# Optimization experiments

Hardware: AMD Instinct MI355X
Metric: run time of the kernel (lower is better)

The kernel has to match this reference:

```python
import jax, jax.numpy as jnp
import numpy as np

B, L, E, H, CDIM = 512, 64, 256, 256, 64
NEG = -1e9  # stand-in for -inf mask fill (keeps grads nan-free; probs underflow to 0)
C_EXPL = 10.0  # tanh_exploration


def setup_inputs():
    key = jax.random.key(0)
    ks = jax.random.split(key, 24)
    rn = lambda k, s: jax.random.normal(k, s, jnp.float32) * 0.05
    return {
        'decoder_input': rn(ks[0], (B, E)),
        'embedded_inputs': rn(ks[1], (L, B, E)),
        'h0': rn(ks[2], (B, H)),
        'c0': rn(ks[3], (B, H)),
        'context': rn(ks[4], (L, B, H)),
        'courier_fea': rn(ks[5], (B, CDIM)),
        'init_mask': jnp.zeros((B, L), dtype=bool),
        # LSTMCell params (torch gate order i,f,g,o)
        'W_ih': rn(ks[6], (4 * H, E)), 'W_hh': rn(ks[7], (4 * H, H)),
        'b_ih': rn(ks[8], (4 * H,)), 'b_hh': rn(ks[9], (4 * H,)),
        # merge_linear
        'Wm': rn(ks[10], (H, H + CDIM)), 'bm': rn(ks[11], (H,)),
        # pointer attention
        'Wq_p': rn(ks[12], (H, H)), 'bq_p': rn(ks[13], (H,)),
        'Wr_p': rn(ks[14], (H, H)), 'br_p': rn(ks[15], (H,)),
        'v_p': rn(ks[16], (H,)),
        # glimpse attention
        'Wq_g': rn(ks[17], (H, H)), 'bq_g': rn(ks[18], (H,)),
        'Wr_g': rn(ks[19], (H, H)), 'br_g': rn(ks[20], (H,)),
        'v_g': rn(ks[21], (H,)),
    }


def _attn_scores(q_lin, e, v, use_tanh):
    # q_lin: [B,H], e: [B,H,L], v: [H] -> u: [B,L]
    u = jnp.einsum('h,bhl->bl', v, jnp.tanh(q_lin[:, :, None] + e))
    return C_EXPL * jnp.tanh(u) if use_tanh else u


def _forward(decoder_input, embedded_inputs, h0, c0, context, courier_fea,
             W_ih, W_hh, b_ih, b_hh, Wm, bm,
             Wq_p, bq_p, Wr_p, br_p, v_p,
             Wq_g, bq_g, Wr_g, br_g, v_g, init_mask):
    Ln, Bn = context.shape[0], context.shape[1]
    # conv1d(kernel=1) projection of encoder refs; constant over steps -> precompute
    e_g = jnp.einsum('oh,lbh->bol', Wr_g, context) + br_g[None, :, None]  # [B,H,L]
    e_p = jnp.einsum('oh,lbh->bol', Wr_p, context) + br_p[None, :, None]
    rows = jnp.arange(Bn)

    def update_mask(mask, sel):
        m = mask.at[rows, sel].set(True)
        all_true = m.all(axis=1)
        return m.at[:, -1].set(jnp.where(all_true, False, m[:, -1]))

    def step(carry, t):
        h, c, mask, idxs, x = carry
        mask = jnp.where(t == 0, mask, update_mask(mask, jnp.clip(idxs, 0)))
        # LSTMCell
        gates = x @ W_ih.T + b_ih + h @ W_hh.T + b_hh
        i_, f_, g_, o_ = jnp.split(gates, 4, axis=1)
        c = jax.nn.sigmoid(f_) * c + jax.nn.sigmoid(i_) * jnp.tanh(g_)
        h = jax.nn.sigmoid(o_) * jnp.tanh(c)
        # merge hidden with courier features
        gl = jnp.concatenate([h, courier_fea], axis=1) @ Wm.T + bm
        # one glimpse (n_glimpses=1), masked
        lg = _attn_scores(gl @ Wq_g.T + bq_g, e_g, v_g, use_tanh=False)
        lg = jnp.where(mask, NEG, lg)
        gl = jnp.einsum('bhl,bl->bh', e_g, jax.nn.softmax(lg, axis=1))
        # pointer logits (C*tanh), masked
        lp = _attn_scores(gl @ Wq_p.T + bq_p, e_p, v_p, use_tanh=True)
        lp = jnp.where(mask, NEG, lp)
        log_p = jax.nn.log_softmax(lp, axis=1)  # [B,L]
        new_idxs = jnp.argmax(log_p, axis=1).astype(jnp.int32)  # greedy decode
        new_x = embedded_inputs[new_idxs, rows, :]  # gather next input [B,E]
        return (h, c, mask, new_idxs, new_x), (log_p, new_idxs)

    init = (h0, c0, init_mask, jnp.full((Bn,), -1, jnp.int32), decoder_input)
    _, (log_ps, sels) = jax.lax.scan(step, init, jnp.arange(Ln))
    return jnp.swapaxes(log_ps, 0, 1), jnp.swapaxes(sels, 0, 1)  # [B,L,L], [B,L]


def reference(decoder_input, embedded_inputs, h0, c0, context, courier_fea, init_mask,
              W_ih, W_hh, b_ih, b_hh, Wm, bm,
              Wq_p, bq_p, Wr_p, br_p, v_p,
              Wq_g, bq_g, Wr_g, br_g, v_g):
    return _forward(decoder_input, embedded_inputs, h0, c0, context, courier_fea,
                    W_ih, W_hh, b_ih, b_hh, Wm, bm,
                    Wq_p, bq_p, Wr_p, br_p, v_p,
                    Wq_g, bq_g, Wr_g, br_g, v_g, init_mask)
```

## Files before the change

### kernel.cpp

```cpp
#include <hip/hip_runtime.h>
#include <cstdint>
#include <cstddef>

#define NEGV -1000000000.0f

__device__ __forceinline__ float fsigm(float x) {
  return 1.0f / (1.0f + __expf(-x));
}
__device__ __forceinline__ float ftanh(float x) {
  x = fminf(x, 30.0f);
  const float e = __expf(2.0f * x);
  return (e - 1.0f) / (e + 1.0f);
}

#define GLOAD_LDS16(gp, lp)                                             \
  __builtin_amdgcn_global_load_lds(                                     \
      (__attribute__((address_space(1))) void*)(gp),                    \
      (__attribute__((address_space(3))) void*)(lp), 16, 0, 0)

__global__ __launch_bounds__(256, 2) void gemm2_k(
    const float* __restrict__ A0, const float* __restrict__ W2,
    const float* __restrict__ b2, float* __restrict__ Cg,
    float* __restrict__ Cp)
{
  __shared__ float As[16][136];
  __shared__ float Ws[2][16][72];
  const int bm = blockIdx.x << 7;
  const int bn = blockIdx.y << 6;
  const int t  = threadIdx.x;
  const int ty = t >> 4, tx = t & 15;
  const int ar = t >> 1, ac = (t & 1) << 3;
  const int wr = t >> 2, wc = (t & 3) << 2;
  const float* arow = A0 + (size_t)(bm + ar) * 256 + ac;
  const float* w0row = W2 + (size_t)(bn + wr) * 256 + wc;
  const float* w1row = W2 + (size_t)(256 + bn + wr) * 256 + wc;
  float acc[2][8][4] = {};
  float4 a0 = *(const float4*)(arow + 0);
  float4 a1 = *(const float4*)(arow + 4);
  float4 wv0 = *(const float4*)(w0row + 0);
  float4 wv1 = *(const float4*)(w1row + 0);
  for (int k0 = 0; k0 < 256; k0 += 16) {
    As[ac + 0][ar] = a0.x; As[ac + 1][ar] = a0.y; As[ac + 2][ar] = a0.z; As[ac + 3][ar] = a0.w;
    As[ac + 4][ar] = a1.x; As[ac + 5][ar] = a1.y; As[ac + 6][ar] = a1.z; As[ac + 7][ar] = a1.w;
    Ws[0][wc + 0][wr] = wv0.x; Ws[0][wc + 1][wr] = wv0.y;
    Ws[0][wc + 2][wr] = wv0.z; Ws[0][wc + 3][wr] = wv0.w;
    Ws[1][wc + 0][wr] = wv1.x; Ws[1][wc + 1][wr] = wv1.y;
    Ws[1][wc + 2][wr] = wv1.z; Ws[1][wc + 3][wr] = wv1.w;
    __syncthreads();
    if (k0 < 240) {
      a0  = *(const float4*)(arow + k0 + 16);
      a1  = *(const float4*)(arow + k0 + 20);
      wv0 = *(const float4*)(w0row + k0 + 16);
      wv1 = *(const float4*)(w1row + k0 + 16);
    }
#pragma unroll
    for (int k = 0; k < 16; ++k) {
      const float4 a0v = *(const float4*)&As[k][ty << 3];
      const float4 a1v = *(const float4*)&As[k][(ty << 3) + 4];
      const float am[8] = {a0v.x, a0v.y, a0v.z, a0v.w, a1v.x, a1v.y, a1v.z, a1v.w};
#pragma unroll
      for (int s = 0; s < 2; ++s) {
        const float4 wv = *(const float4*)&Ws[s][k][tx << 2];
#pragma unroll
        for (int i = 0; i < 8; ++i) {
          acc[s][i][0] += am[i] * wv.x;
          acc[s][i][1] += am[i] * wv.y;
          acc[s][i][2] += am[i] * wv.z;
          acc[s][i][3] += am[i] * wv.w;
        }
      }
    }
    __syncthreads();
  }
  const int cn = bn + (tx << 2);
  const float4 bg = *(const float4*)(b2 + cn);
  const float4 bp = *(const float4*)(b2 + 256 + cn);
#pragma unroll
  for (int i = 0; i < 8; ++i) {
    const size_t row = ((size_t)(bm + (ty << 3) + i)) << 8;
    float4 o;
    o.x = acc[0][i][0] + bg.x; o.y = acc[0][i][1] + bg.y;
    o.z = acc[0][i][2] + bg.z; o.w = acc[0][i][3] + bg.w;
    *(float4*)(Cg + row + cn) = o;
    o.x = acc[1][i][0] + bp.x; o.y = acc[1][i][1] + bp.y;
    o.z = acc[1][i][2] + bp.z; o.w = acc[1][i][3] + bp.w;
    *(float4*)(Cp + row + cn) = o;
  }
}

__global__ __launch_bounds__(256) void gates_lstm_k(
    const float* __restrict__ x, const float* __restrict__ hin,
    const float* __restrict__ Wcat, const float* __restrict__ bcat,
    const float* __restrict__ cin, float* __restrict__ cnew,
    float* __restrict__ hnew)
{
  __shared__ __align__(16) float As[16][36];
  __shared__ __align__(16) float Ws[32][68];
  const int bn = blockIdx.x << 6;
  const int bm = blockIdx.y << 4;
  const int t  = threadIdx.x;
  const int ty = t >> 4, tx = t & 15;
  const int ar = t >> 4, ak = (t & 15) << 1;
  const int wr = t >> 2, wk = (t & 3) << 3;
  const float* wrow = Wcat + ((size_t)(bn + wr) << 9);
  const int arow = bm + ar;
  float acc0 = 0.f, acc1 = 0.f, acc2 = 0.f, acc3 = 0.f;
  for (int k0 = 0; k0 < 512; k0 += 32) {
    const int kk = k0 + ak;
    float2 av;
    if (kk < 256) av = *(const float2*)(x   + ((size_t)arow << 8) + kk);
    else          av = *(const float2*)(hin + ((size_t)arow << 8) + (kk - 256));
    const float4 w0 = *(const float4*)(wrow + k0 + wk);
    const float4 w1 = *(const float4*)(wrow + k0 + wk + 4);
    *(float2*)&As[ar][ak] = av;
    Ws[wk + 0][wr] = w0.x; Ws[wk + 1][wr] = w0.y; Ws[wk + 2][wr] = w0.z; Ws[wk + 3][wr] = w0.w;
    Ws[wk + 4][wr] = w1.x; Ws[wk + 5][wr] = w1.y; Ws[wk + 6][wr] = w1.z; Ws[wk + 7][wr] = w1.w;
    __syncthreads();
#pragma unroll
    for (int k = 0; k < 32; ++k) {
      const float a  = As[ty][k];
      const float4 w = *(const float4*)&Ws[k][tx << 2];
      acc0 += a * w.x; acc1 += a * w.y; acc2 += a * w.z; acc3 += a * w.w;
    }
    __syncthreads();
  }
  const float4 bb = *(const float4*)(bcat + bn + (tx << 2));
  const int jc = (bn >> 2) + tx;
  const int m  = bm + ty;
  const float ig = fsigm(acc0 + bb.x);
  const float fg = fsigm(acc1 + bb.y);
  const float gg = ftanh(acc2 + bb.z);
  const float og = fsigm(acc3 + bb.w);
  const float c  = fg * cin[(m << 8) + jc] + ig * gg;
  const float h  = og * ftanh(c);
  cnew[(m << 8) + jc] = c;
  hnew[(m << 8) + jc] = h;
}

__global__ __launch_bounds__(512) void step_attn_k(
    const float* __restrict__ h, const float* __restrict__ e2g,
    const float* __restrict__ e2p, const float* __restrict__ Wq1T4,
    const float* __restrict__ Wqp4, const float* __restrict__ qcour,
    const float* __restrict__ bqp, const float* __restrict__ vg,
    const float* __restrict__ vp, unsigned long long* __restrict__ mask,
    int* __restrict__ idxb, const float* __restrict__ emb,
    float* __restrict__ out_logp, float* __restrict__ out_sel,
    float* __restrict__ xb, int t)
{
  const int b = blockIdx.x, tid = threadIdx.x;
  __shared__ __align__(16) float hs[256], qgs[256], qps[256], gls[256];
  __shared__ __align__(16) float vgs[256], vps[256];
  __shared__ __align__(16) float glp[8][256];
  __shared__ __align__(16) float eps[64][256];
  __shared__ float us[64], mxs[8], zws[8];
  __shared__ unsigned long long ms;
  __shared__ int bsel;
  float* part = &glp[0][0];
  if (tid < 256) {
    hs[tid]  = h[(b << 8) + tid];
    vgs[tid] = vg[tid];
    vps[tid] = vp[tid];
  }
  if (tid == 0) {
    unsigned long long m = mask[b];
    if (t > 0) {
      int s = idxb[b]; if (s < 0) s = 0;
      m |= (1ULL << s);
      if (m == ~0ULL) m &= ~(1ULL << 63);
      mask[b] = m;
    }
    ms = m;
  }
  __syncthreads();
  const unsigned long long mm = ms;
  const int w = tid >> 6, lane = tid & 63;
  const int o = tid & 255, kh = tid >> 8;

  {
    const float* gb = e2g + ((size_t)b << 8) + (lane << 2);
#pragma unroll
    for (int li = 0; li < 8; ++li) {
      const int l = (w << 3) + li;
      GLOAD_LDS16(gb + ((size_t)l << 17), &eps[l][0]);
    }
  }

  {
    float acc = (kh == 0) ? qcour[(b << 8) + o] : 0.f;
    const float4* wp = (const float4*)Wq1T4 + o;
    const int kc0 = kh << 5;
#pragma unroll 8
    for (int kc = kc0; kc < kc0 + 32; ++kc) {
      const float4 wv = wp[kc << 8];
      const float4 h4 = *(const float4*)&hs[kc << 2];
      acc += wv.x * h4.x + wv.y * h4.y + wv.z * h4.z + wv.w * h4.w;
    }
    part[tid] = acc;
  }
  __syncthreads();
  if (tid < 256) qgs[tid] = part[tid] + part[tid + 256];
  __syncthreads();

  {
    const float4 q4 = *(const float4*)&qgs[lane << 2];
    const float4 v4 = *(const float4*)&vgs[lane << 2];
    float g0 = 0.f, g1 = 0.f, g2 = 0.f, g3 = 0.f;
    float mxw = -1e30f, zw = 0.f;
    for (int li = 0; li < 8; ++li) {
      const int l = (w << 3) + li;
      const float4 e4 = *(const float4*)&eps[l][lane << 2];
      float s = v4.x * ftanh(q4.x + e4.x) + v4.y * ftanh(q4.y + e4.y)
              + v4.z * ftanh(q4.z + e4.z) + v4.w * ftanh(q4.w + e4.w);
#pragma unroll
      for (int off = 32; off; off >>= 1) s += __shfl_xor(s, off, 64);
      if (!((mm >> l) & 1ULL)) {
        const float nm   = fmaxf(mxw, s);
        const float corr = __expf(mxw - nm);
        const float wl   = __expf(s - nm);
        zw = zw * corr + wl;
        g0 = g0 * corr + wl * e4.x; g1 = g1 * corr + wl * e4.y;
        g2 = g2 * corr + wl * e4.z; g3 = g3 * corr + wl * e4.w;
        mxw = nm;
      }
    }
    glp[w][(lane << 2) + 0] = g0; glp[w][(lane << 2) + 1] = g1;
    glp[w][(lane << 2) + 2] = g2; glp[w][(lane << 2) + 3] = g3;
    if (lane == 0) { mxs[w] = mxw; zws[w] = zw; }
  }
  __syncthreads();
  if (tid < 256) {
    float MX = mxs[0];
#pragma unroll
    for (int ww = 1; ww < 8; ++ww) MX = fmaxf(MX, mxs[ww]);
    float Z = 0.f, go = 0.f;
#pragma unroll
    for (int ww = 0; ww < 8; ++ww) {
      const float sc = __expf(mxs[ww] - MX);
      Z  += sc * zws[ww];
      go += sc * glp[ww][tid];
    }
    gls[tid] = go / Z;
  }
  {
    const float* gb = e2p + ((size_t)b << 8) + (lane << 2);
#pragma unroll
    for (int li = 0; li < 8; ++li) {
      const int l = (w << 3) + li;
      GLOAD_LDS16(gb + ((size_t)l << 17), &eps[l][0]);
    }
  }
  __syncthreads();

  {
    float acc = (kh == 0) ? bqp[o] : 0.f;
    const float4* wp = (const float4*)Wqp4 + o;
    const int kc0 = kh << 5;
#pragma unroll 8
    for (int kc = kc0; kc < kc0 + 32; ++kc) {
      const float4 wv = wp[kc << 8];
      const float4 h4 = *(const float4*)&gls[kc << 2];
      acc += wv.x * h4.x + wv.y * h4.y + wv.z * h4.z + wv.w * h4.w;
    }
    part[tid] = acc;
  }
  __syncthreads();
  if (tid < 256) qps[tid] = part[tid] + part[tid + 256];
  __syncthreads();

  {
    const float4 q4 = *(const float4*)&qps[lane << 2];
    const float4 v4 = *(const float4*)&vps[lane << 2];
    for (int li = 0; li < 8; ++li) {
      const int l = (w << 3) + li;
      const float4 e4 = *(const float4*)&eps[l][lane << 2];
      float s = v4.x * ftanh(q4.x + e4.x) + v4.y * ftanh(q4.y + e4.y)
              + v4.z * ftanh(q4.z + e4.z) + v4.w * ftanh(q4.w + e4.w);
#pragma unroll
      for (int off = 32; off; off >>= 1) s += __shfl_xor(s, off, 64);
      if (lane == 0) us[l] = ((mm >> l) & 1ULL) ? NEGV : 10.0f * ftanh(s);
    }
  }
  __syncthreads();
  if (tid < 64) {
    const float xv = us[tid];
    float mx = xv;
#pragma unroll
    for (int off = 32; off; off >>= 1) mx = fmaxf(mx, __shfl_xor(mx, off, 64));
    const float sh = xv - mx;
    const float ev = __expf(sh);
    float sum = ev;
#pragma unroll
    for (int off = 32; off; off >>= 1) sum += __shfl_xor(sum, off, 64);
    const float lp = sh - __logf(sum);
    out_logp[((size_t)b << 12) + (t << 6) + tid] = lp;
    float bv = lp; int bi = tid;
#pragma unroll
    for (int off = 32; off; off >>= 1) {
      const float ov = __shfl_xor(bv, off, 64);
      const int   oi = __shfl_xor(bi, off, 64);
      if (ov > bv || (ov == bv && oi < bi)) { bv = ov; bi = oi; }
    }
    if (tid == 0) { idxb[b] = bi; out_sel[(b << 6) + t] = (float)bi; bsel = bi; }
  }
  __syncthreads();
  if (tid < 256) xb[(b << 8) + tid] = emb[(((size_t)(bsel << 9) + b) << 8) + tid];
}

__global__ __launch_bounds__(256) void init_k(
    const float* __restrict__ dec, const float* __restrict__ h0,
    const float* __restrict__ c0, float* __restrict__ xb,
    float* __restrict__ hb, float* __restrict__ cb,
    unsigned long long* __restrict__ mask, int* __restrict__ idxb)
{
  const int i = blockIdx.x * 256 + threadIdx.x;
  xb[i] = dec[i]; hb[i] = h0[i]; cb[i] = c0[i];
  if (i < 512) { mask[i] = 0ULL; idxb[i] = -1; }
}

__global__ __launch_bounds__(256) void prep_wcat_k(
    const float* __restrict__ Wih, const float* __restrict__ Whh,
    const float* __restrict__ bih, const float* __restrict__ bhh,
    float* __restrict__ Wcat, float* __restrict__ bcat)
{
  const int id = blockIdx.x * 256 + threadIdx.x;
  const int n = id >> 9, k = id & 511;
  const int r = ((n & 3) << 8) + (n >> 2);
  Wcat[id] = (k < 256) ? Wih[(r << 8) + k] : Whh[(r << 8) + (k - 256)];
  if (id < 1024) {
    const int rr = ((id & 3) << 8) + (id >> 2);
    bcat[id] = bih[rr] + bhh[rr];
  }
}

__global__ __launch_bounds__(256) void prep_wfused_k(
    const float* __restrict__ Wqg, const float* __restrict__ Wm,
    const float* __restrict__ bm, const float* __restrict__ bqg,
    float* __restrict__ Wf, float* __restrict__ bf)
{
  const int id = blockIdx.x * 256 + threadIdx.x;
  const int o = id / 320, j = id % 320;
  float acc = 0.f;
  for (int tt = 0; tt < 256; ++tt) acc += Wqg[(o << 8) + tt] * Wm[tt * 320 + j];
  Wf[id] = acc;
  if (id < 256) {
    float a2 = 0.f;
    for (int tt = 0; tt < 256; ++tt) a2 += Wqg[(id << 8) + tt] * bm[tt];
    bf[id] = a2 + bqg[id];
  }
}

__global__ __launch_bounds__(256) void prep_wq1t4_k(
    const float* __restrict__ Wf, float* __restrict__ Wq1T4)
{
  const int id = blockIdx.x * 256 + threadIdx.x;
  const int k = id >> 8, o = id & 255;
  Wq1T4[((k >> 2) << 10) + (o << 2) + (k & 3)] = Wf[o * 320 + k];
}

__global__ __launch_bounds__(256) void prep_wqp4_k(
    const float* __restrict__ Wqp, float* __restrict__ Wqp4)
{
  const int id = blockIdx.x * 256 + threadIdx.x;
  const int k = id >> 8, o = id & 255;
  Wqp4[((k >> 2) << 10) + (o << 2) + (k & 3)] = Wqp[(o << 8) + k];
}

__global__ __launch_bounds__(256) void prep_qcour_k(
    const float* __restrict__ Wf, const float* __restrict__ bf,
    const float* __restrict__ cour, float* __restrict__ qcour)
{
  const int b = blockIdx.x, o = threadIdx.x;
  __shared__ float cs[64];
  if (o < 64) cs[o] = cour[(b << 6) + o];
  __syncthreads();
  float acc = bf[o];
#pragma unroll 8
  for (int k = 0; k < 64; ++k) acc += Wf[o * 320 + 256 + k] * cs[k];
  qcour[(b << 8) + o] = acc;
}

__global__ __launch_bounds__(256) void prep_w2copy_k(
    const float* __restrict__ Wrg, const float* __restrict__ Wrp,
    const float* __restrict__ brg, const float* __restrict__ brp,
    float* __restrict__ W2, float* __restrict__ b2)
{
  const int id = blockIdx.x * 256 + threadIdx.x;
  W2[id] = (id < 65536) ? Wrg[id] : Wrp[id - 65536];
  if (id < 256) b2[id] = brg[id];
  else if (id < 512) b2[id] = brp[id - 256];
}

extern "C" void kernel_launch(void* const* d_in, const int* in_sizes, int n_in,
                              void* d_out, int out_size, void* d_ws, size_t ws_size,
                              hipStream_t stream)
{
  const float* dec   = (const float*)d_in[0];
  const float* emb   = (const float*)d_in[1];
  const float* h0    = (const float*)d_in[2];
  const float* c0    = (const float*)d_in[3];
  const float* ctxin = (const float*)d_in[4];
  const float* cour  = (const float*)d_in[5];
  const float* Wih   = (const float*)d_in[7];
  const float* Whh   = (const float*)d_in[8];
  const float* bih   = (const float*)d_in[9];
  const float* bhh   = (const float*)d_in[10];
  const float* Wm    = (const float*)d_in[11];
  const float* bm    = (const float*)d_in[12];
  const float* Wqp   = (const float*)d_in[13];
  const float* bqp   = (const float*)d_in[14];
  const float* Wrp   = (const float*)d_in[15];
  const float* brp   = (const float*)d_in[16];
  const float* vp    = (const float*)d_in[17];
  const float* Wqg   = (const float*)d_in[18];
  const float* bqg   = (const float*)d_in[19];
  const float* Wrg   = (const float*)d_in[20];
  const float* brg   = (const float*)d_in[21];
  const float* vg    = (const float*)d_in[22];

  float* ws = (float*)d_ws;
  float* e2g    = ws + 0;
  float* e2p    = ws + 8388608;
  float* W2     = ws + 16777216;
  float* b2     = ws + 16908288;
  float* Wcat   = ws + 16908800;
  float* bcat   = ws + 17433088;
  float* Wfused = ws + 17434112;
  float* bfused = ws + 17516032;
  float* Wq1T4  = ws + 17516288;
  float* Wqp4   = ws + 17581824;
  float* qcour  = ws + 17647360;
  float* hb0    = ws + 17778432;
  float* hb1    = ws + 17909504;
  float* cb0    = ws + 18040576;
  float* cb1    = ws + 18171648;
  float* xb     = ws + 18302720;
  unsigned long long* maskb = (unsigned long long*)(ws + 18433792);
  int* idxb     = (int*)(ws + 18434816);

  float* out_logp = (float*)d_out;
  float* out_sel  = (float*)d_out + 2097152;

  init_k<<<512, 256, 0, stream>>>(dec, h0, c0, xb, hb0, cb0, maskb, idxb);
  prep_wcat_k<<<2048, 256, 0, stream>>>(Wih, Whh, bih, bhh, Wcat, bcat);
  prep_wfused_k<<<320, 256, 0, stream>>>(Wqg, Wm, bm, bqg, Wfused, bfused);
  prep_wq1t4_k<<<256, 256, 0, stream>>>(Wfused, Wq1T4);
  prep_wqp4_k<<<256, 256, 0, stream>>>(Wqp, Wqp4);
  prep_qcour_k<<<512, 256, 0, stream>>>(Wfused, bfused, cour, qcour);
  prep_w2copy_k<<<512, 256, 0, stream>>>(Wrg, Wrp, brg, brp, W2, b2);
  gemm2_k<<<dim3(256, 4), 256, 0, stream>>>(ctxin, W2, b2, e2g, e2p);

  for (int t = 0; t < 64; ++t) {
    float* hcur = (t & 1) ? hb1 : hb0;
    float* hnew = (t & 1) ? hb0 : hb1;
    float* ccur = (t & 1) ? cb1 : cb0;
    float* cnew = (t & 1) ? cb0 : cb1;
    gates_lstm_k<<<dim3(16, 32), 256, 0, stream>>>(xb, hcur, Wcat, bcat,
                                                   ccur, cnew, hnew);
    step_attn_k<<<512, 512, 0, stream>>>(hnew, e2g, e2p, Wq1T4, Wqp4, qcour,
                                         bqp, vg, vp, maskb, idxb, emb,
                                         out_logp, out_sel, xb, t);
  }
}
```

Measured before the change: 3.383 ms.

## Load attention refs directly from global and skip masked positions

Drops the 64 KB LDS staging buffer for the glimpse and pointer reference tensors and reads each float4 directly from global memory inside the scoring loops. Positions already masked are skipped entirely, so their loads, tanh work and shuffle reductions are not executed. The much smaller shared footprint allows more blocks per CU. The cost is that the async bulk prefetch no longer overlaps the query matvec, so load latency sits inside the loop.

```diff
diff --git a/kernel.cpp b/kernel.cpp
--- a/kernel.cpp
+++ b/kernel.cpp
@@ -12,11 +12,6 @@
   const float e = __expf(2.0f * x);
   return (e - 1.0f) / (e + 1.0f);
 }
-
-#define GLOAD_LDS16(gp, lp)                                             \
-  __builtin_amdgcn_global_load_lds(                                     \
-      (__attribute__((address_space(1))) void*)(gp),                    \
-      (__attribute__((address_space(3))) void*)(lp), 16, 0, 0)
 
 __global__ __launch_bounds__(256, 2) void gemm2_k(
     const float* __restrict__ A0, const float* __restrict__ W2,
@@ -151,11 +146,10 @@
   __shared__ __align__(16) float hs[256], qgs[256], qps[256], gls[256];
   __shared__ __align__(16) float vgs[256], vps[256];
   __shared__ __align__(16) float glp[8][256];
-  __shared__ __align__(16) float eps[64][256];
+  __shared__ __align__(16) float part[512];
   __shared__ float us[64], mxs[8], zws[8];
   __shared__ unsigned long long ms;
   __shared__ int bsel;
-  float* part = &glp[0][0];
   if (tid < 256) {
     hs[tid]  = h[(b << 8) + tid];
     vgs[tid] = vg[tid];
@@ -175,15 +169,6 @@
   const unsigned long long mm = ms;
   const int w = tid >> 6, lane = tid & 63;
   const int o = tid & 255, kh = tid >> 8;
-
-  {
-    const float* gb = e2g + ((size_t)b << 8) + (lane << 2);
-#pragma unroll
-    for (int li = 0; li < 8; ++li) {
-      const int l = (w << 3) + li;
-      GLOAD_LDS16(gb + ((size_t)l << 17), &eps[l][0]);
-    }
-  }
 
   {
     float acc = (kh == 0) ? qcour[(b << 8) + o] : 0.f;
@@ -204,16 +189,18 @@
   {
     const float4 q4 = *(const float4*)&qgs[lane << 2];
     const float4 v4 = *(const float4*)&vgs[lane << 2];
+    const float* ebase = e2g + ((size_t)b << 8) + (lane << 2);
     float g0 = 0.f, g1 = 0.f, g2 = 0.f, g3 = 0.f;
     float mxw = -1e30f, zw = 0.f;
     for (int li = 0; li < 8; ++li) {
       const int l = (w << 3) + li;
-      const float4 e4 = *(const float4*)&eps[l][lane << 2];
+      if ((mm >> l) & 1ULL) continue;
+      const float4 e4 = *(const float4*)(ebase + ((size_t)l << 17));
       float s = v4.x * ftanh(q4.x + e4.x) + v4.y * ftanh(q4.y + e4.y)
               + v4.z * ftanh(q4.z + e4.z) + v4.w * ftanh(q4.w + e4.w);
 #pragma unroll
       for (int off = 32; off; off >>= 1) s += __shfl_xor(s, off, 64);
-      if (!((mm >> l) & 1ULL)) {
+      {
         const float nm   = fmaxf(mxw, s);
         const float corr = __expf(mxw - nm);
         const float wl   = __expf(s - nm);
@@ -240,14 +227,6 @@
       go += sc * glp[ww][tid];
     }
     gls[tid] = go / Z;
-  }
-  {
-    const float* gb = e2p + ((size_t)b << 8) + (lane << 2);
-#pragma unroll
-    for (int li = 0; li < 8; ++li) {
-      const int l = (w << 3) + li;
-      GLOAD_LDS16(gb + ((size_t)l << 17), &eps[l][0]);
-    }
   }
   __syncthreads();
 
@@ -270,14 +249,19 @@
   {
     const float4 q4 = *(const float4*)&qps[lane << 2];
     const float4 v4 = *(const float4*)&vps[lane << 2];
+    const float* ebase = e2p + ((size_t)b << 8) + (lane << 2);
     for (int li = 0; li < 8; ++li) {
       const int l = (w << 3) + li;
-      const float4 e4 = *(const float4*)&eps[l][lane << 2];
+      if ((mm >> l) & 1ULL) {
+        if (lane == 0) us[l] = NEGV;
+        continue;
+      }
+      const float4 e4 = *(const float4*)(ebase + ((size_t)l << 17));
       float s = v4.x * ftanh(q4.x + e4.x) + v4.y * ftanh(q4.y + e4.y)
               + v4.z * ftanh(q4.z + e4.z) + v4.w * ftanh(q4.w + e4.w);
 #pragma unroll
       for (int off = 32; off; off >>= 1) s += __shfl_xor(s, off, 64);
-      if (lane == 0) us[l] = ((mm >> l) & 1ULL) ? NEGV : 10.0f * ftanh(s);
+      if (lane == 0) us[l] = 10.0f * ftanh(s);
     }
   }
   __syncthreads();
```

Result: faster. 2.975 ms (-12.1%).
